# Kernel tuning notes

Hardware: AMD Instinct MI355X
Metric: run time of the kernel (lower is better)

## Reference

```python
import jax, jax.numpy as jnp
import numpy as np

B, T, H, D = 2, 1024, 8, 64
C = H * D            # 512 = n_embd = heads*head_dim
M = 32768            # external memory size
TOPK = 32
SCALE = D ** -0.5
EPS_NORM = 1e-12


def _layernorm(x, w, b, eps=1e-5):
    mu = jnp.mean(x, axis=-1, keepdims=True)
    var = jnp.var(x, axis=-1, keepdims=True)
    return (x - mu) * jax.lax.rsqrt(var + eps) * w + b


def _l2norm(x):
    n = jnp.linalg.norm(x, axis=-1, keepdims=True)
    return x / jnp.maximum(n, EPS_NORM)


def setup_inputs() -> dict:
    key = jax.random.key(0)
    ks = jax.random.split(key, 12)
    s = C ** -0.5
    return {
        "x": jax.random.normal(ks[0], (B, T, C), jnp.float32),
        "memory_kv": jax.random.normal(ks[1], (B, M, 2, C), jnp.float32),
        "ln_w": jnp.ones((C,), jnp.float32),
        "ln_b": jnp.zeros((C,), jnp.float32),
        "Wq": jax.random.normal(ks[2], (C, C), jnp.float32) * s,
        "bq": jnp.zeros((C,), jnp.float32),
        "Wk": jax.random.normal(ks[3], (C, C), jnp.float32) * s,
        "bk": jnp.zeros((C,), jnp.float32),
        "Wv": jax.random.normal(ks[4], (C, C), jnp.float32) * s,
        "bv": jnp.zeros((C,), jnp.float32),
        "Wo": jax.random.normal(ks[5], (C, C), jnp.float32) * s,
        "bo": jnp.zeros((C,), jnp.float32),
        "gate_bias": jax.random.normal(ks[6], (H, 1, 1), jnp.float32),
    }


def reference(x, memory_kv, ln_w, ln_b, Wq, bq, Wk, bk, Wv, bv, Wo, bo, gate_bias):
    xn = _layernorm(x, ln_w, ln_b)
    q = _l2norm(xn @ Wq + bq)           # [B,T,C], F.normalize(dim=-1)
    k = _l2norm(xn @ Wk + bk)
    v = xn @ Wv + bv

    qh = q.reshape(B, T, H, D).transpose(0, 2, 1, 3)   # b h t d
    kh = k.reshape(B, T, H, D).transpose(0, 2, 1, 3)
    vh = v.reshape(B, T, H, D).transpose(0, 2, 1, 3)

    # local causal attention
    qk = jnp.einsum('bhid,bhjd->bhij', qh, kh) * SCALE
    causal = jnp.triu(jnp.ones((T, T), bool), k=1)
    qk = jnp.where(causal, -jnp.inf, qk)
    attn = jax.nn.softmax(qk, axis=-1)
    qkv = attn @ vh                                     # b h t d

    # kNN retrieval: top-k inner product of flat queries vs stored keys
    q_flat = q                                          # b t C (normalized)
    mem_keys = memory_kv[:, :, 0]                       # b M C
    scores = jnp.einsum('btc,bmc->btm', q_flat, mem_keys)
    _, idx = jax.lax.top_k(scores, TOPK)                # b t k
    # gather retrieved kv: [b, t, k, 2, C]
    mem = jnp.take_along_axis(memory_kv[:, None], idx[:, :, :, None, None], axis=2)
    mem_k = mem[..., 0, :].reshape(B, T, TOPK, H, D).transpose(0, 3, 1, 2, 4)  # b h t k d
    mem_v = mem[..., 1, :].reshape(B, T, TOPK, H, D).transpose(0, 3, 1, 2, 4)

    mem_qk = jnp.einsum('bhtd,bhtkd->bhtk', qh, mem_k) * SCALE
    mem_attn = jax.nn.softmax(mem_qk, axis=-1)
    mem_qkv = jnp.einsum('bhtk,bhtkd->bhtd', mem_attn, mem_v)

    combined = mem_qkv * gate_bias + qkv * (1.0 - gate_bias)  # gate_bias [H,1,1]
    combined = combined.transpose(0, 2, 1, 3).reshape(B, T, C)
    out = combined @ Wo + bo

    current_kv = jnp.stack((k, v), axis=-2)             # b t 2 C (normalized keys)
    return out, current_kv
```

## Files before the change

### kernel.cpp

```cpp
#include <hip/hip_runtime.h>
#include <hip/hip_bf16.h>

#define B_ 2
#define T_ 1024
#define H_ 8
#define D_ 64
#define C_ 512
#define M_ 32768
#define TOPK_ 32
#define NCAND_ 64
#define SCALE_ 0.125f
#define QSCALE_ 360.0f
#define KSCALE_ 24.0f
#define OSCALE_ 20.0f

typedef unsigned short u16;
typedef float    f32x2  __attribute__((ext_vector_type(2)));
typedef float    f32x4  __attribute__((ext_vector_type(4)));
typedef __bf16   bf16x8 __attribute__((ext_vector_type(8)));
typedef u16      u16x4  __attribute__((ext_vector_type(4)));
typedef int      i32x4  __attribute__((ext_vector_type(4)));
typedef unsigned char u8x4 __attribute__((ext_vector_type(4)));

__device__ __forceinline__ u16 f2bf(float f) {
  __hip_bfloat16 b = __float2bfloat16(f);
  u16 u; __builtin_memcpy(&u, &b, 2); return u;
}

__device__ __forceinline__ unsigned char q8(float v, float scale) {
  int iv = (int)rintf(v * scale);
  iv = iv > 127 ? 127 : (iv < -127 ? -127 : iv);
  return (unsigned char)(signed char)iv;
}

__device__ __forceinline__ void gl_lds16(const void* g, void* l) {
  __builtin_amdgcn_global_load_lds(
      (const __attribute__((address_space(1))) void*)g,
      (__attribute__((address_space(3))) void*)l, 16, 0, 0);
}

__global__ __launch_bounds__(256) void wtrans_kernel(
    const float* __restrict__ W0, const float* __restrict__ W1,
    const float* __restrict__ W2, u16* __restrict__ WT) {
  __shared__ u16 tl[32][33];
  int z = blockIdx.z;
  const float* W = (z == 0) ? W0 : (z == 1) ? W1 : W2;
  u16* dst = WT + (size_t)z * C_ * C_;
  int n0 = blockIdx.x * 32, k0 = blockIdx.y * 32;
  int tx = threadIdx.x, ty = threadIdx.y;
#pragma unroll
  for (int i = 0; i < 4; ++i) {
    int k = k0 + ty + i * 8;
    tl[ty + i * 8][tx] = f2bf(W[(size_t)k * C_ + n0 + tx]);
  }
  __syncthreads();
#pragma unroll
  for (int i = 0; i < 4; ++i) {
    int nn = ty + i * 8;
    dst[(size_t)(n0 + nn) * C_ + k0 + tx] = tl[tx][nn];
  }
}

__global__ __launch_bounds__(256) void prep_keys_kernel(
    const float* __restrict__ mem, char* __restrict__ ki) {
  const int n4 = B_ * M_ * C_ / 4;
  for (int i = blockIdx.x * 256 + threadIdx.x; i < n4; i += gridDim.x * 256) {
    int row = i >> 7;
    int c4 = i & 127;
    f32x4 v = *(const f32x4*)(mem + ((size_t)row * 1024) + c4 * 4);
    u8x4 o;
    o[0] = q8(v[0], KSCALE_); o[1] = q8(v[1], KSCALE_);
    o[2] = q8(v[2], KSCALE_); o[3] = q8(v[3], KSCALE_);
    *(u8x4*)((unsigned char*)ki + (size_t)i * 4) = o;
  }
}

__global__ __launch_bounds__(256) void ln_kernel(
    const float* __restrict__ x, const float* __restrict__ w,
    const float* __restrict__ bia, u16* __restrict__ xn, float* __restrict__ xnf) {
  int row = blockIdx.x * 4 + (threadIdx.x >> 6);
  int lane = threadIdx.x & 63;
  const float* xr = x + (size_t)row * C_;
  f32x4 v0 = *(const f32x4*)(xr + lane * 4);
  f32x4 v1 = *(const f32x4*)(xr + 256 + lane * 4);
  float s = v0[0] + v0[1] + v0[2] + v0[3] + v1[0] + v1[1] + v1[2] + v1[3];
  float q = v0[0]*v0[0]+v0[1]*v0[1]+v0[2]*v0[2]+v0[3]*v0[3]
          + v1[0]*v1[0]+v1[1]*v1[1]+v1[2]*v1[2]+v1[3]*v1[3];
#pragma unroll
  for (int m = 1; m < 64; m <<= 1) { s += __shfl_xor(s, m); q += __shfl_xor(q, m); }
  float mean = s * (1.0f / C_);
  float var  = q * (1.0f / C_) - mean * mean;
  float rs = rsqrtf(var + 1e-5f);
  u16x4 o0, o1;
  f32x4 f0, f1;
#pragma unroll
  for (int e = 0; e < 4; ++e) {
    int c = lane * 4 + e;
    f0[e] = (v0[e] - mean) * rs * w[c] + bia[c];
    o0[e] = f2bf(f0[e]);
    int c2 = 256 + lane * 4 + e;
    f1[e] = (v1[e] - mean) * rs * w[c2] + bia[c2];
    o1[e] = f2bf(f1[e]);
  }
  *(u16x4*)(xn + (size_t)row * C_ + lane * 4) = o0;
  *(u16x4*)(xn + (size_t)row * C_ + 256 + lane * 4) = o1;
  *(f32x4*)(xnf + (size_t)row * C_ + lane * 4) = f0;
  *(f32x4*)(xnf + (size_t)row * C_ + 256 + lane * 4) = f1;
}

__global__ __launch_bounds__(256) void gemm_f32(
    const float* __restrict__ A, const float* __restrict__ Bw,
    const float* __restrict__ bias, float* __restrict__ Cout) {
  __shared__ float As[64][33];
  __shared__ float Bs[32][64];
  int tid = threadIdx.x;
  int tx = tid & 15, ty = tid >> 4;
  int r0 = blockIdx.x * 64, c0 = blockIdx.y * 64;
  f32x4 acc[4];
#pragma unroll
  for (int i = 0; i < 4; ++i) acc[i] = f32x4{0.f, 0.f, 0.f, 0.f};
  for (int kt = 0; kt < 16; ++kt) {
    int k0 = kt * 32;
#pragma unroll
    for (int i2 = 0; i2 < 2; ++i2) {
      int idx = i2 * 256 + tid;
      int arow = idx >> 3, ac = idx & 7;
      f32x4 av = *(const f32x4*)(A + (size_t)(r0 + arow) * 512 + k0 + ac * 4);
      As[arow][ac * 4 + 0] = av[0]; As[arow][ac * 4 + 1] = av[1];
      As[arow][ac * 4 + 2] = av[2]; As[arow][ac * 4 + 3] = av[3];
      int krow = idx >> 4, cc = idx & 15;
      f32x4 bv = *(const f32x4*)(Bw + (size_t)(k0 + krow) * 512 + c0 + cc * 4);
      *(f32x4*)(&Bs[krow][cc * 4]) = bv;
    }
    __syncthreads();
#pragma unroll
    for (int kk = 0; kk < 32; ++kk) {
      f32x4 bv = *(const f32x4*)(&Bs[kk][tx * 4]);
#pragma unroll
      for (int i = 0; i < 4; ++i) {
        float av = As[ty * 4 + i][kk];
        acc[i] += av * bv;
      }
    }
    __syncthreads();
  }
  f32x4 bb = *(const f32x4*)(bias + c0 + tx * 4);
#pragma unroll
  for (int i = 0; i < 4; ++i)
    *(f32x4*)(Cout + (size_t)(r0 + ty * 4 + i) * 512 + c0 + tx * 4) = acc[i] + bb;
}

__global__ __launch_bounds__(256) void gemm128(
    const u16* __restrict__ A, long aBS,
    const u16* __restrict__ Bt, long bBS,
    float* __restrict__ Cf, long cBS,
    const float* __restrict__ bias, const float* __restrict__ bias2, int ldc) {
  __shared__ __align__(16) u16 As[128 * 64];
  __shared__ __align__(16) u16 Bs[128 * 64];
  const int tid = threadIdx.x;
  const int lane = tid & 63, w = tid >> 6;
  const int wm = w >> 1, wn = w & 1;
  const int z = blockIdx.z;
  const u16* Ab = A + (size_t)z * aBS + (size_t)blockIdx.x * 128 * 512;
  const u16* Bb = Bt + (size_t)z * bBS + (size_t)blockIdx.y * 128 * 512;

  f32x4 acc[4][4];
#pragma unroll
  for (int i = 0; i < 4; ++i)
#pragma unroll
    for (int j = 0; j < 4; ++j) acc[i][j] = f32x4{0.f, 0.f, 0.f, 0.f};

  for (int kt = 0; kt < 8; ++kt) {
    const u16* Akt = Ab + kt * 64;
    const u16* Bkt = Bb + kt * 64;
#pragma unroll
    for (int it = 0; it < 4; ++it) {
      int slot = it * 256 + tid;
      int rr = slot >> 3, ss = slot & 7;
      int q = ss ^ (rr & 7);
      gl_lds16(Akt + (size_t)rr * 512 + q * 8, (char*)As + slot * 16);
      gl_lds16(Bkt + (size_t)rr * 512 + q * 8, (char*)Bs + slot * 16);
    }
    __syncthreads();
#pragma unroll
    for (int kk = 0; kk < 2; ++kk) {
      bf16x8 av[4], bv[4];
#pragma unroll
      for (int i = 0; i < 4; ++i) {
        int blk = kk * 4 + (lane >> 4);
        int ra = wm * 64 + i * 16 + (lane & 15);
        av[i] = *(const bf16x8*)((const char*)As + ra * 128 + ((blk ^ (ra & 7)) << 4));
        int rb = wn * 64 + i * 16 + (lane & 15);
        bv[i] = *(const bf16x8*)((const char*)Bs + rb * 128 + ((blk ^ (rb & 7)) << 4));
      }
#pragma unroll
      for (int mi = 0; mi < 4; ++mi)
#pragma unroll
        for (int ni = 0; ni < 4; ++ni)
          acc[mi][ni] = __builtin_amdgcn_mfma_f32_16x16x32_bf16(av[mi], bv[ni], acc[mi][ni], 0, 0, 0);
    }
    __syncthreads();
  }
  const float* bi = (z == 1 && bias2) ? bias2 : bias;
  const long cbase = (long)z * cBS;
  const int rsub = (lane >> 4) * 4;
  const long row0 = (long)blockIdx.x * 128 + wm * 64;
  const int col00 = wn * 64 + (lane & 15) + (int)blockIdx.y * 128;
#pragma unroll
  for (int mi = 0; mi < 4; ++mi)
#pragma unroll
    for (int rg = 0; rg < 4; ++rg) {
      long row = row0 + mi * 16 + rsub + rg;
#pragma unroll
      for (int ni = 0; ni < 4; ++ni) {
        int col = col00 + ni * 16;
        float bb = bi ? bi[col] : 0.0f;
        Cf[cbase + row * (long)ldc + col] = acc[mi][ni][rg] + bb;
      }
    }
}

__global__ __launch_bounds__(256) void gemm_sc8(
    const char* __restrict__ A, const char* __restrict__ Bt, char* __restrict__ sc8) {
  __shared__ __align__(16) char As[128 * 64];
  __shared__ __align__(16) char Bs[128 * 64];
  const int tid = threadIdx.x;
  const int lane = tid & 63, w = tid >> 6;
  const int wm = w >> 1, wn = w & 1;
  const int p = blockIdx.x;
  const int z = p >> 11;
  const int q_ = p & 2047;
  const int r = (q_ >> 3) & 7;
  const int c = ((q_ >> 6) << 3) | (q_ & 7);
  const char* Ab = A + (size_t)z * T_ * C_ + (size_t)r * 128 * 512;
  const char* Bb = Bt + (size_t)z * M_ * C_ + (size_t)c * 128 * 512;

  i32x4 acc[4][4];
#pragma unroll
  for (int i = 0; i < 4; ++i)
#pragma unroll
    for (int j = 0; j < 4; ++j) acc[i][j] = i32x4{0, 0, 0, 0};

  for (int kt = 0; kt < 8; ++kt) {
    const char* Akt = Ab + kt * 64;
    const char* Bkt = Bb + kt * 64;
#pragma unroll
    for (int it = 0; it < 2; ++it) {
      int slot = it * 256 + tid;
      int rr = slot >> 2, cw = slot & 3;
      int ch = cw ^ (rr & 3);
      gl_lds16(Akt + (size_t)rr * 512 + ch * 16, As + slot * 16);
      gl_lds16(Bkt + (size_t)rr * 512 + ch * 16, Bs + slot * 16);
    }
    __syncthreads();
    i32x4 av[4], bv[4];
#pragma unroll
    for (int i = 0; i < 4; ++i) {
      int ra = wm * 64 + i * 16 + (lane & 15);
      av[i] = *(const i32x4*)(As + ra * 64 + (((lane >> 4) ^ (ra & 3)) << 4));
      int rb = wn * 64 + i * 16 + (lane & 15);
      bv[i] = *(const i32x4*)(Bs + rb * 64 + (((lane >> 4) ^ (rb & 3)) << 4));
    }
#pragma unroll
    for (int mi = 0; mi < 4; ++mi)
#pragma unroll
      for (int ni = 0; ni < 4; ++ni)
        acc[mi][ni] = __builtin_amdgcn_mfma_i32_16x16x64_i8(av[mi], bv[ni], acc[mi][ni], 0, 0, 0);
    __syncthreads();
  }
  const int rsub = (lane >> 4) * 4;
  const long row0 = (long)r * 128 + wm * 64;
  const int col00 = c * 128 + wn * 64 + (lane & 15);
  char* base = sc8 + (size_t)z * T_ * M_;
  const float osc = OSCALE_ / (QSCALE_ * KSCALE_);
#pragma unroll
  for (int mi = 0; mi < 4; ++mi)
#pragma unroll
    for (int rg = 0; rg < 4; ++rg) {
      long row = row0 + mi * 16 + rsub + rg;
#pragma unroll
      for (int ni = 0; ni < 4; ++ni) {
        int iv = (int)rintf((float)acc[mi][ni][rg] * osc);
        iv = iv > 127 ? 127 : (iv < -127 ? -127 : iv);
        base[row * (long)M_ + col00 + ni * 16] = (char)iv;
      }
    }
}

__global__ __launch_bounds__(256) void postproc_kernel(
    const float* __restrict__ qraw, const float* __restrict__ kraw,
    const float* __restrict__ vraw, float* __restrict__ qf,
    u16* __restrict__ qb, u16* __restrict__ kb, char* __restrict__ qi,
    float* __restrict__ kvout) {
  int row = blockIdx.x * 4 + (threadIdx.x >> 6);
  int lane = threadIdx.x & 63;
  size_t rb_ = (size_t)row * C_;
  f32x4 a0 = *(const f32x4*)(qraw + rb_ + lane * 4);
  f32x4 a1 = *(const f32x4*)(qraw + rb_ + 256 + lane * 4);
  float ss = a0[0]*a0[0]+a0[1]*a0[1]+a0[2]*a0[2]+a0[3]*a0[3]
           + a1[0]*a1[0]+a1[1]*a1[1]+a1[2]*a1[2]+a1[3]*a1[3];
#pragma unroll
  for (int m = 1; m < 64; m <<= 1) ss += __shfl_xor(ss, m);
  float rn = 1.0f / fmaxf(sqrtf(ss), 1e-12f);
  f32x4 q0 = a0 * rn, q1 = a1 * rn;
  *(f32x4*)(qf + rb_ + lane * 4) = q0;
  *(f32x4*)(qf + rb_ + 256 + lane * 4) = q1;
  u16x4 t0, t1;
#pragma unroll
  for (int e = 0; e < 4; ++e) { t0[e] = f2bf(q0[e]); t1[e] = f2bf(q1[e]); }
  *(u16x4*)(qb + rb_ + lane * 4) = t0;
  *(u16x4*)(qb + rb_ + 256 + lane * 4) = t1;
  u8x4 i0, i1;
#pragma unroll
  for (int e = 0; e < 4; ++e) { i0[e] = q8(q0[e], QSCALE_); i1[e] = q8(q1[e], QSCALE_); }
  *(u8x4*)((unsigned char*)qi + rb_ + lane * 4) = i0;
  *(u8x4*)((unsigned char*)qi + rb_ + 256 + lane * 4) = i1;
  f32x4 b0 = *(const f32x4*)(kraw + rb_ + lane * 4);
  f32x4 b1 = *(const f32x4*)(kraw + rb_ + 256 + lane * 4);
  float sk = b0[0]*b0[0]+b0[1]*b0[1]+b0[2]*b0[2]+b0[3]*b0[3]
           + b1[0]*b1[0]+b1[1]*b1[1]+b1[2]*b1[2]+b1[3]*b1[3];
#pragma unroll
  for (int m = 1; m < 64; m <<= 1) sk += __shfl_xor(sk, m);
  float rk = 1.0f / fmaxf(sqrtf(sk), 1e-12f);
  f32x4 k0 = b0 * rk, k1 = b1 * rk;
  size_t kvb = (size_t)row * (2 * C_);
  *(f32x4*)(kvout + kvb + lane * 4) = k0;
  *(f32x4*)(kvout + kvb + 256 + lane * 4) = k1;
#pragma unroll
  for (int e = 0; e < 4; ++e) { t0[e] = f2bf(k0[e]); t1[e] = f2bf(k1[e]); }
  *(u16x4*)(kb + rb_ + lane * 4) = t0;
  *(u16x4*)(kb + rb_ + 256 + lane * 4) = t1;
  f32x4 c0 = *(const f32x4*)(vraw + rb_ + lane * 4);
  f32x4 c1 = *(const f32x4*)(vraw + rb_ + 256 + lane * 4);
  *(f32x4*)(kvout + kvb + C_ + lane * 4) = c0;
  *(f32x4*)(kvout + kvb + C_ + 256 + lane * 4) = c1;
}

__global__ __launch_bounds__(256) void vtrans_kernel(
    const float* __restrict__ vraw, u16* __restrict__ vT) {
  __shared__ u16 tile[64][65];
  int tt = blockIdx.x, h = blockIdx.y, b = blockIdx.z;
  int tx = threadIdx.x, ty = threadIdx.y;
#pragma unroll
  for (int i = 0; i < 8; ++i) {
    int t = tt * 64 + ty + i * 8;
    const float* src = vraw + (size_t)(b * T_ + t) * C_ + h * 64;
    tile[ty + i * 8][tx] = f2bf(src[tx]);
    tile[ty + i * 8][tx + 32] = f2bf(src[tx + 32]);
  }
  __syncthreads();
#pragma unroll
  for (int i = 0; i < 8; ++i) {
    int d = ty + i * 8;
    u16* dst = vT + ((size_t)((b * H_ + h) * 64 + d)) * T_ + tt * 64;
    dst[tx] = tile[tx][d];
    dst[tx + 32] = tile[tx + 32][d];
  }
}

__global__ __launch_bounds__(256) void attn_kernel(
    const u16* __restrict__ qb, const u16* __restrict__ kb,
    const u16* __restrict__ vT, float* __restrict__ o) {
  __shared__ __align__(16) u16 Ks[128 * 64];
  __shared__ __align__(16) u16 Vs[64 * 128];
  __shared__ __align__(16) u16 Ps[4][16 * 128];
  int tid = threadIdx.x, lane = tid & 63, w = tid >> 6;
  int it = blockIdx.x, h = blockIdx.y, b = blockIdx.z;
  int t0 = it * 64;
  bf16x8 aq[2];
#pragma unroll
  for (int kk = 0; kk < 2; ++kk) {
    int row = t0 + w * 16 + (lane & 15);
    aq[kk] = *(const bf16x8*)(qb + (size_t)(b * T_ + row) * C_ + h * 64 + kk * 32 + (lane >> 4) * 8);
  }
  f32x4 accO[4];
  float denp[4];
#pragma unroll
  for (int j = 0; j < 4; ++j) { accO[j] = f32x4{0.f,0.f,0.f,0.f}; denp[j] = 0.f; }

  int ntiles = it / 2 + 1;
  for (int jt = 0; jt < ntiles; ++jt) {
    int j0 = jt * 128;
#pragma unroll
    for (int i2 = 0; i2 < 4; ++i2) {
      int slot = i2 * 256 + tid;
      int rr = slot >> 3, ssw = slot & 7;
      int q = ssw ^ (rr & 7);
      gl_lds16(kb + (size_t)(b * T_ + j0 + rr) * C_ + h * 64 + q * 8, (char*)Ks + slot * 16);
    }
#pragma unroll
    for (int i2 = 0; i2 < 4; ++i2) {
      int slot = i2 * 256 + tid;
      int rr = slot >> 4, ssw = slot & 15;
      int q = ssw ^ (rr & 15);
      gl_lds16(vT + ((size_t)((b * H_ + h) * 64 + rr)) * T_ + j0 + q * 8, (char*)Vs + slot * 16);
    }
    __syncthreads();
    f32x4 s[8];
#pragma unroll
    for (int ni = 0; ni < 8; ++ni) s[ni] = f32x4{0.f,0.f,0.f,0.f};
#pragma unroll
    for (int kk = 0; kk < 2; ++kk) {
      bf16x8 bk[8];
#pragma unroll
      for (int ni = 0; ni < 8; ++ni) {
        int rbi = ni * 16 + (lane & 15);
        int blk = kk * 4 + (lane >> 4);
        bk[ni] = *(const bf16x8*)((const char*)Ks + rbi * 128 + ((blk ^ (rbi & 7)) << 4));
      }
#pragma unroll
      for (int ni = 0; ni < 8; ++ni)
        s[ni] = __builtin_amdgcn_mfma_f32_16x16x32_bf16(aq[kk], bk[ni], s[ni], 0, 0, 0);
    }
#pragma unroll
    for (int ni = 0; ni < 8; ++ni)
#pragma unroll
      for (int rg = 0; rg < 4; ++rg) {
        int qrow = t0 + w * 16 + (lane >> 4) * 4 + rg;
        int kvcol = j0 + ni * 16 + (lane & 15);
        float sv = s[ni][rg] * SCALE_;
        float p = (kvcol <= qrow) ? __expf(sv) : 0.0f;
        denp[rg] += p;
        int qk = (lane >> 4) * 4 + rg;
        int kvl = ni * 16 + (lane & 15);
        int blk2 = kvl >> 3;
        *(u16*)((char*)Ps[w] + qk * 256 + ((blk2 ^ qk) << 4) + (kvl & 7) * 2) = f2bf(p);
      }
#pragma unroll
    for (int kk2 = 0; kk2 < 4; ++kk2) {
      bf16x8 ap, bvv[4];
      int blk = kk2 * 4 + (lane >> 4);
      int rq = lane & 15;
      ap = *(const bf16x8*)((const char*)Ps[w] + rq * 256 + ((blk ^ rq) << 4));
#pragma unroll
      for (int nd = 0; nd < 4; ++nd) {
        int rd = nd * 16 + (lane & 15);
        bvv[nd] = *(const bf16x8*)((const char*)Vs + rd * 256 + ((blk ^ (rd & 15)) << 4));
      }
#pragma unroll
      for (int nd = 0; nd < 4; ++nd)
        accO[nd] = __builtin_amdgcn_mfma_f32_16x16x32_bf16(ap, bvv[nd], accO[nd], 0, 0, 0);
    }
    __syncthreads();
  }
  float den[4];
#pragma unroll
  for (int rg = 0; rg < 4; ++rg) {
    float d = denp[rg];
    d += __shfl_xor(d, 1); d += __shfl_xor(d, 2);
    d += __shfl_xor(d, 4); d += __shfl_xor(d, 8);
    den[rg] = d;
  }
#pragma unroll
  for (int nd = 0; nd < 4; ++nd)
#pragma unroll
    for (int rg = 0; rg < 4; ++rg) {
      int row = t0 + w * 16 + (lane >> 4) * 4 + rg;
      int d = nd * 16 + (lane & 15);
      o[(size_t)(b * T_ + row) * C_ + h * 64 + d] = accO[nd][rg] / den[rg];
    }
}

__global__ __launch_bounds__(256) void topk_tail_kernel(
    const char* __restrict__ scores, const float* __restrict__ qf,
    const float* __restrict__ mem, const float* __restrict__ attn,
    const float* __restrict__ gate, u16* __restrict__ comb) {
  int row = blockIdx.x, b = row >> 10;
  int tid = threadIdx.x, lane = tid & 63, w = tid >> 6;
  __shared__ unsigned candKey[256];
  __shared__ float qL[512];
  __shared__ float sL[NCAND_];
  __shared__ float sHh[NCAND_][8];
  __shared__ int cL[NCAND_];
  __shared__ int wIdx[TOPK_];
  __shared__ float eL[TOPK_][8];
  qL[tid] = qf[(size_t)row * C_ + tid];
  qL[256 + tid] = qf[(size_t)row * C_ + 256 + tid];
  const unsigned char* s = (const unsigned char*)scores + (size_t)row * M_;
  unsigned c[8];
#pragma unroll
  for (int i = 0; i < 8; ++i) c[i] = 0;
  for (int i2 = 0; i2 < 16; ++i2) {
    int base = i2 * 2048 + tid * 8;
    uint2 v = *(const uint2*)(s + base);
#pragma unroll
    for (int e = 0; e < 8; ++e) {
      unsigned byte = (e < 4) ? ((v.x >> (8 * e)) & 0xFF) : ((v.y >> (8 * (e - 4))) & 0xFF);
      unsigned key = byte ^ 0x80u;
      unsigned cmb = (key << 15) | (unsigned)(32767 - (base + e));
      if (cmb > c[7]) {
        c[7] = cmb;
#pragma unroll
        for (int ss = 7; ss > 0; --ss) {
          if (c[ss] > c[ss - 1]) { unsigned t = c[ss - 1]; c[ss - 1] = c[ss]; c[ss] = t; }
        }
      }
    }
  }
  for (int r = 0; r < 64; ++r) {
    unsigned bb = c[0];
#pragma unroll
    for (int m = 1; m < 64; m <<= 1) {
      unsigned o = __shfl_xor(bb, m);
      bb = (o > bb) ? o : bb;
    }
    if (lane == 0) candKey[w * 64 + r] = bb;
    if (c[0] == bb) {
#pragma unroll
      for (int ss = 0; ss < 7; ++ss) c[ss] = c[ss + 1];
      c[7] = 0;
    }
  }
  __syncthreads();
  {
    unsigned my = candKey[tid];
    int rank = 0;
    for (int j = 0; j < 256; ++j) rank += (candKey[j] > my);
    if (rank < NCAND_) cL[rank] = 32767 - (int)(my & 32767u);
  }
  __syncthreads();
#pragma unroll 4
  for (int i = 0; i < 16; ++i) {
    int cdx = w * 16 + i;
    const float* mrow = mem + ((size_t)(b * M_ + cL[cdx])) * 1024;
    f32x4 k0 = *(const f32x4*)(mrow + lane * 8);
    f32x4 k1 = *(const f32x4*)(mrow + lane * 8 + 4);
    float p = qL[lane*8+0]*k0[0] + qL[lane*8+1]*k0[1] + qL[lane*8+2]*k0[2] + qL[lane*8+3]*k0[3]
            + qL[lane*8+4]*k1[0] + qL[lane*8+5]*k1[1] + qL[lane*8+6]*k1[2] + qL[lane*8+7]*k1[3];
    p += __shfl_xor(p, 1); p += __shfl_xor(p, 2); p += __shfl_xor(p, 4);
    if ((lane & 7) == 0) sHh[cdx][lane >> 3] = p;
    float pf = p;
    pf += __shfl_xor(pf, 8); pf += __shfl_xor(pf, 16); pf += __shfl_xor(pf, 32);
    if (lane == 0) sL[cdx] = pf;
  }
  __syncthreads();
  if (tid < NCAND_) {
    float sv = sL[tid]; int id = cL[tid];
    int rank = 0;
#pragma unroll
    for (int j = 0; j < NCAND_; ++j) {
      float sj = sL[j];
      rank += (sj > sv) || (sj == sv && cL[j] < id);
    }
    if (rank < TOPK_) {
      wIdx[rank] = id;
#pragma unroll
      for (int h = 0; h < 8; ++h)
        eL[rank][h] = __expf(sHh[tid][h] * SCALE_);
    }
  }
  __syncthreads();
  int h2 = tid >> 5, dp = tid & 31;
  float num0 = 0.f, num1 = 0.f, den = 0.f;
#pragma unroll 8
  for (int k = 0; k < TOPK_; ++k) {
    float wgt = eL[k][h2];
    const float* vrow = mem + ((size_t)(b * M_ + wIdx[k])) * 1024 + 512;
    f32x2 vv = *(const f32x2*)(vrow + h2 * 64 + dp * 2);
    num0 += wgt * vv[0];
    num1 += wgt * vv[1];
    den += wgt;
  }
  float g = gate[h2];
  int c0 = h2 * 64 + dp * 2;
  float a0 = attn[(size_t)row * C_ + c0];
  float a1 = attn[(size_t)row * C_ + c0 + 1];
  u16 o0 = f2bf(g * (num0 / den) + (1.0f - g) * a0);
  u16 o1 = f2bf(g * (num1 / den) + (1.0f - g) * a1);
  *(unsigned*)(comb + (size_t)row * C_ + c0) = (unsigned)o0 | ((unsigned)o1 << 16);
}

extern "C" void kernel_launch(void* const* d_in, const int* in_sizes, int n_in,
                              void* d_out, int out_size, void* d_ws, size_t ws_size,
                              hipStream_t stream) {
  const float* x    = (const float*)d_in[0];
  const float* mem  = (const float*)d_in[1];
  const float* lnw  = (const float*)d_in[2];
  const float* lnb  = (const float*)d_in[3];
  const float* Wq   = (const float*)d_in[4];
  const float* bq   = (const float*)d_in[5];
  const float* Wk   = (const float*)d_in[6];
  const float* bk   = (const float*)d_in[7];
  const float* Wv   = (const float*)d_in[8];
  const float* bv   = (const float*)d_in[9];
  const float* Wo   = (const float*)d_in[10];
  const float* bo   = (const float*)d_in[11];
  const float* gate = (const float*)d_in[12];
  float* out   = (float*)d_out;
  float* kvout = out + (size_t)B_ * T_ * C_;

  size_t off = 0;
  auto alloc = [&](size_t bytes) {
    char* r = (char*)d_ws + off;
    off += (bytes + 255) & ~(size_t)255;
    return r;
  };
  u16*      WT   = (u16*)alloc(3ull * C_ * C_ * 2);
  char*     ki   = (char*)alloc((size_t)B_ * M_ * C_);
  u16*      xn   = (u16*)alloc((size_t)B_ * T_ * C_ * 2);
  float*    xnf  = (float*)alloc((size_t)B_ * T_ * C_ * 4);
  float*    qraw = (float*)alloc((size_t)B_ * T_ * C_ * 4);
  float*    kvraw= (float*)alloc(2ull * B_ * T_ * C_ * 4);
  float*    kraw = kvraw;
  float*    vraw = kvraw + (size_t)B_ * T_ * C_;
  float*    qf   = (float*)alloc((size_t)B_ * T_ * C_ * 4);
  u16*      qb   = (u16*)alloc((size_t)B_ * T_ * C_ * 2);
  u16*      kb   = (u16*)alloc((size_t)B_ * T_ * C_ * 2);
  char*     qi   = (char*)alloc((size_t)B_ * T_ * C_);
  u16*      vT   = (u16*)alloc((size_t)B_ * T_ * C_ * 2);
  float*    attn = (float*)alloc((size_t)B_ * T_ * C_ * 4);
  char*     sc8  = (char*)alloc((size_t)B_ * T_ * M_);
  u16*      comb = (u16*)alloc((size_t)B_ * T_ * C_ * 2);
  if (off > ws_size) return;

  wtrans_kernel<<<dim3(16, 16, 3), dim3(32, 8), 0, stream>>>(Wk, Wv, Wo, WT);
  prep_keys_kernel<<<8192, 256, 0, stream>>>(mem, ki);
  ln_kernel<<<512, 256, 0, stream>>>(x, lnw, lnb, xn, xnf);
  gemm_f32<<<dim3(32, 8), 256, 0, stream>>>(xnf, Wq, bq, qraw);
  gemm128<<<dim3(16, 4, 2), 256, 0, stream>>>(xn, 0, WT, (long)C_ * C_,
                                              kvraw, (long)B_ * T_ * C_, bk, bv, C_);
  postproc_kernel<<<512, 256, 0, stream>>>(qraw, kraw, vraw, qf, qb, kb, qi, kvout);
  vtrans_kernel<<<dim3(16, 8, 2), dim3(32, 8), 0, stream>>>(vraw, vT);
  attn_kernel<<<dim3(16, 8, 2), 256, 0, stream>>>(qb, kb, vT, attn);
  gemm_sc8<<<4096, 256, 0, stream>>>(qi, ki, sc8);
  topk_tail_kernel<<<2048, 256, 0, stream>>>(sc8, qf, mem, attn, gate, comb);
  gemm128<<<dim3(16, 4, 1), 256, 0, stream>>>(comb, 0, WT + 2 * C_ * C_, 0,
                                              out, 0, bo, nullptr, C_);
}
```

Measured before the change: 326.3 us.

## Merge causal attention and int8 score GEMM into one launch

Combines the local causal attention kernel and the int8 memory-score GEMM into a single kernel whose block index chooses which body to run, with a shared 48KB LDS pool. The intent is to let the 256 attention blocks run alongside the 4096 score-GEMM blocks and to remove one launch boundary and the tail idle time of the small attention grid. In exchange, every block now reserves 48KB of LDS, which can lower occupancy for the GEMM blocks that used only 16KB before, and register usage becomes the maximum of the two bodies.

```diff
diff --git a/kernel.cpp b/kernel.cpp
--- a/kernel.cpp
+++ b/kernel.cpp
@@ -220,73 +220,6 @@
     }
 }
 
-__global__ __launch_bounds__(256) void gemm_sc8(
-    const char* __restrict__ A, const char* __restrict__ Bt, char* __restrict__ sc8) {
-  __shared__ __align__(16) char As[128 * 64];
-  __shared__ __align__(16) char Bs[128 * 64];
-  const int tid = threadIdx.x;
-  const int lane = tid & 63, w = tid >> 6;
-  const int wm = w >> 1, wn = w & 1;
-  const int p = blockIdx.x;
-  const int z = p >> 11;
-  const int q_ = p & 2047;
-  const int r = (q_ >> 3) & 7;
-  const int c = ((q_ >> 6) << 3) | (q_ & 7);
-  const char* Ab = A + (size_t)z * T_ * C_ + (size_t)r * 128 * 512;
-  const char* Bb = Bt + (size_t)z * M_ * C_ + (size_t)c * 128 * 512;
-
-  i32x4 acc[4][4];
-#pragma unroll
-  for (int i = 0; i < 4; ++i)
-#pragma unroll
-    for (int j = 0; j < 4; ++j) acc[i][j] = i32x4{0, 0, 0, 0};
-
-  for (int kt = 0; kt < 8; ++kt) {
-    const char* Akt = Ab + kt * 64;
-    const char* Bkt = Bb + kt * 64;
-#pragma unroll
-    for (int it = 0; it < 2; ++it) {
-      int slot = it * 256 + tid;
-      int rr = slot >> 2, cw = slot & 3;
-      int ch = cw ^ (rr & 3);
-      gl_lds16(Akt + (size_t)rr * 512 + ch * 16, As + slot * 16);
-      gl_lds16(Bkt + (size_t)rr * 512 + ch * 16, Bs + slot * 16);
-    }
-    __syncthreads();
-    i32x4 av[4], bv[4];
-#pragma unroll
-    for (int i = 0; i < 4; ++i) {
-      int ra = wm * 64 + i * 16 + (lane & 15);
-      av[i] = *(const i32x4*)(As + ra * 64 + (((lane >> 4) ^ (ra & 3)) << 4));
-      int rb = wn * 64 + i * 16 + (lane & 15);
-      bv[i] = *(const i32x4*)(Bs + rb * 64 + (((lane >> 4) ^ (rb & 3)) << 4));
-    }
-#pragma unroll
-    for (int mi = 0; mi < 4; ++mi)
-#pragma unroll
-      for (int ni = 0; ni < 4; ++ni)
-        acc[mi][ni] = __builtin_amdgcn_mfma_i32_16x16x64_i8(av[mi], bv[ni], acc[mi][ni], 0, 0, 0);
-    __syncthreads();
-  }
-  const int rsub = (lane >> 4) * 4;
-  const long row0 = (long)r * 128 + wm * 64;
-  const int col00 = c * 128 + wn * 64 + (lane & 15);
-  char* base = sc8 + (size_t)z * T_ * M_;
-  const float osc = OSCALE_ / (QSCALE_ * KSCALE_);
-#pragma unroll
-  for (int mi = 0; mi < 4; ++mi)
-#pragma unroll
-    for (int rg = 0; rg < 4; ++rg) {
-      long row = row0 + mi * 16 + rsub + rg;
-#pragma unroll
-      for (int ni = 0; ni < 4; ++ni) {
-        int iv = (int)rintf((float)acc[mi][ni][rg] * osc);
-        iv = iv > 127 ? 127 : (iv < -127 ? -127 : iv);
-        base[row * (long)M_ + col00 + ni * 16] = (char)iv;
-      }
-    }
-}
-
 __global__ __launch_bounds__(256) void postproc_kernel(
     const float* __restrict__ qraw, const float* __restrict__ kraw,
     const float* __restrict__ vraw, float* __restrict__ qf,
@@ -358,14 +291,16 @@
   }
 }
 
-__global__ __launch_bounds__(256) void attn_kernel(
+
+__device__ __forceinline__ void attn_body(char* pool, int p,
     const u16* __restrict__ qb, const u16* __restrict__ kb,
     const u16* __restrict__ vT, float* __restrict__ o) {
-  __shared__ __align__(16) u16 Ks[128 * 64];
-  __shared__ __align__(16) u16 Vs[64 * 128];
-  __shared__ __align__(16) u16 Ps[4][16 * 128];
+  u16* Ks = (u16*)pool;
+  u16* Vs = (u16*)(pool + 16384);
+  char* PsBase = pool + 32768;
   int tid = threadIdx.x, lane = tid & 63, w = tid >> 6;
-  int it = blockIdx.x, h = blockIdx.y, b = blockIdx.z;
+  int it = p & 15, h = (p >> 4) & 7, b = p >> 7;
+  char* PsW = PsBase + w * 4096;
   int t0 = it * 64;
   bf16x8 aq[2];
 #pragma unroll
@@ -419,19 +354,19 @@
         int qrow = t0 + w * 16 + (lane >> 4) * 4 + rg;
         int kvcol = j0 + ni * 16 + (lane & 15);
         float sv = s[ni][rg] * SCALE_;
-        float p = (kvcol <= qrow) ? __expf(sv) : 0.0f;
-        denp[rg] += p;
+        float pp = (kvcol <= qrow) ? __expf(sv) : 0.0f;
+        denp[rg] += pp;
         int qk = (lane >> 4) * 4 + rg;
         int kvl = ni * 16 + (lane & 15);
         int blk2 = kvl >> 3;
-        *(u16*)((char*)Ps[w] + qk * 256 + ((blk2 ^ qk) << 4) + (kvl & 7) * 2) = f2bf(p);
+        *(u16*)(PsW + qk * 256 + ((blk2 ^ qk) << 4) + (kvl & 7) * 2) = f2bf(pp);
       }
 #pragma unroll
     for (int kk2 = 0; kk2 < 4; ++kk2) {
       bf16x8 ap, bvv[4];
       int blk = kk2 * 4 + (lane >> 4);
       int rq = lane & 15;
-      ap = *(const bf16x8*)((const char*)Ps[w] + rq * 256 + ((blk ^ rq) << 4));
+      ap = *(const bf16x8*)(PsW + rq * 256 + ((blk ^ rq) << 4));
 #pragma unroll
       for (int nd = 0; nd < 4; ++nd) {
         int rd = nd * 16 + (lane & 15);
@@ -459,6 +394,83 @@
       int d = nd * 16 + (lane & 15);
       o[(size_t)(b * T_ + row) * C_ + h * 64 + d] = accO[nd][rg] / den[rg];
     }
+}
+
+__device__ __forceinline__ void sc8_body(char* pool, int p,
+    const char* __restrict__ A, const char* __restrict__ Bt, char* __restrict__ sc8) {
+  char* As = pool;
+  char* Bs = pool + 8192;
+  const int tid = threadIdx.x;
+  const int lane = tid & 63, w = tid >> 6;
+  const int wm = w >> 1, wn = w & 1;
+  const int z = p >> 11;
+  const int q_ = p & 2047;
+  const int r = (q_ >> 3) & 7;
+  const int c = ((q_ >> 6) << 3) | (q_ & 7);
+  const char* Ab = A + (size_t)z * T_ * C_ + (size_t)r * 128 * 512;
+  const char* Bb = Bt + (size_t)z * M_ * C_ + (size_t)c * 128 * 512;
+
+  i32x4 acc[4][4];
+#pragma unroll
+  for (int i = 0; i < 4; ++i)
+#pragma unroll
+    for (int j = 0; j < 4; ++j) acc[i][j] = i32x4{0, 0, 0, 0};
+
+  for (int kt = 0; kt < 8; ++kt) {
+    const char* Akt = Ab + kt * 64;
+    const char* Bkt = Bb + kt * 64;
+#pragma unroll
+    for (int it = 0; it < 2; ++it) {
+      int slot = it * 256 + tid;
+      int rr = slot >> 2, cw = slot & 3;
+      int ch = cw ^ (rr & 3);
+      gl_lds16(Akt + (size_t)rr * 512 + ch * 16, As + slot * 16);
+      gl_lds16(Bkt + (size_t)rr * 512 + ch * 16, Bs + slot * 16);
+    }
+    __syncthreads();
+    i32x4 av[4], bv[4];
+#pragma unroll
+    for (int i = 0; i < 4; ++i) {
+      int ra = wm * 64 + i * 16 + (lane & 15);
+      av[i] = *(const i32x4*)(As + ra * 64 + (((lane >> 4) ^ (ra & 3)) << 4));
+      int rb = wn * 64 + i * 16 + (lane & 15);
+      bv[i] = *(const i32x4*)(Bs + rb * 64 + (((lane >> 4) ^ (rb & 3)) << 4));
+    }
+#pragma unroll
+    for (int mi = 0; mi < 4; ++mi)
+#pragma unroll
+      for (int ni = 0; ni < 4; ++ni)
+        acc[mi][ni] = __builtin_amdgcn_mfma_i32_16x16x64_i8(av[mi], bv[ni], acc[mi][ni], 0, 0, 0);
+    __syncthreads();
+  }
+  const int rsub = (lane >> 4) * 4;
+  const long row0 = (long)r * 128 + wm * 64;
+  const int col00 = c * 128 + wn * 64 + (lane & 15);
+  char* base = sc8 + (size_t)z * T_ * M_;
+  const float osc = OSCALE_ / (QSCALE_ * KSCALE_);
+#pragma unroll
+  for (int mi = 0; mi < 4; ++mi)
+#pragma unroll
+    for (int rg = 0; rg < 4; ++rg) {
+      long row = row0 + mi * 16 + rsub + rg;
+#pragma unroll
+      for (int ni = 0; ni < 4; ++ni) {
+        int iv = (int)rintf((float)acc[mi][ni][rg] * osc);
+        iv = iv > 127 ? 127 : (iv < -127 ? -127 : iv);
+        base[row * (long)M_ + col00 + ni * 16] = (char)iv;
+      }
+    }
+}
+
+__global__ __launch_bounds__(256) void fatL4(
+    const u16* __restrict__ qb, const u16* __restrict__ kb,
+    const u16* __restrict__ vT, float* __restrict__ attn,
+    const char* __restrict__ qi, const char* __restrict__ ki,
+    char* __restrict__ sc8) {
+  __shared__ __align__(16) char pool[49152];
+  int p = blockIdx.x;
+  if (p < 256) attn_body(pool, p, qb, kb, vT, attn);
+  else sc8_body(pool, p - 256, qi, ki, sc8);
 }
 
 __global__ __launch_bounds__(256) void topk_tail_kernel(
@@ -621,8 +633,7 @@
                                               kvraw, (long)B_ * T_ * C_, bk, bv, C_);
   postproc_kernel<<<512, 256, 0, stream>>>(qraw, kraw, vraw, qf, qb, kb, qi, kvout);
   vtrans_kernel<<<dim3(16, 8, 2), dim3(32, 8), 0, stream>>>(vraw, vT);
-  attn_kernel<<<dim3(16, 8, 2), 256, 0, stream>>>(qb, kb, vT, attn);
-  gemm_sc8<<<4096, 256, 0, stream>>>(qi, ki, sc8);
+  fatL4<<<256 + 4096, 256, 0, stream>>>(qb, kb, vT, attn, qi, ki, sc8);
   topk_tail_kernel<<<2048, 256, 0, stream>>>(sc8, qf, mem, attn, gate, comb);
   gemm128<<<dim3(16, 4, 1), 256, 0, stream>>>(comb, 0, WT + 2 * C_ * C_, 0,
                                               out, 0, bo, nullptr, C_);
```

Result: no change. 324.8 us (-0.5%).
